# Performance work log

Measured on AMD Instinct MI355X. Metric: run time of the kernel, lower is better.

## Reference

```python
import jax, jax.numpy as jnp
import numpy as np

MARGIN = 0.2
EPS = 1e-12  # guards sqrt(0) (self-distance diagonal); sqrt(1e-12)=1e-6, negligible


def setup_inputs() -> dict:
    key = jax.random.key(0)
    n, m, d = 62, 256, 256          # parts, batch (32 ids x 8 samples), feat dim
    k_per_class = 8                 # positives per anchor (incl. self)
    feature = jax.random.normal(key, (n, m, d), dtype=jnp.float32)
    # structured labels required by the boolean_mask/reshape trick: equal counts per anchor
    label = jnp.broadcast_to(jnp.arange(m, dtype=jnp.int64) // k_per_class, (n, m))
    return {"feature": feature, "label": label, "num_pos": k_per_class}


def reference(feature, label, num_pos):
    n, m, d = feature.shape
    num_neg = m - num_pos
    hp_mask = label[:, :, None] == label[:, None, :]  # (n,m,m) same-id mask (incl. self)

    # batched pairwise euclidean distance
    x2 = jnp.sum(feature * feature, axis=2, keepdims=True)                   # (n,m,1)
    d2 = x2 + jnp.swapaxes(x2, 1, 2) - 2.0 * jnp.einsum('nid,njd->nij', feature, feature)
    dist = jnp.sqrt(jnp.maximum(d2, 0.0) + EPS)                              # (n,m,m)
    mean_dist = jnp.mean(dist)

    # stable argsort of mask: in-set entries (0) come first, in original column order,
    # exactly matching tf.boolean_mask row-major extraction + reshape.
    pos_idx = jnp.argsort((~hp_mask).astype(jnp.int32), axis=2)[:, :, :num_pos]
    neg_idx = jnp.argsort(hp_mask.astype(jnp.int32), axis=2)[:, :, :num_neg]
    pos_d = jnp.take_along_axis(dist, pos_idx, axis=2)  # (n,m,num_pos)
    neg_d = jnp.take_along_axis(dist, neg_idx, axis=2)  # (n,m,num_neg)

    # hard mining
    hard_loss = jax.nn.relu(MARGIN + jnp.max(pos_d, axis=2) - jnp.min(neg_d, axis=2))
    hard_loss_metric_mean = jnp.mean(hard_loss, axis=1)  # (n,)

    # full mining: all (pos, neg) pairs -> (n, m, num_pos, num_neg)
    full = jax.nn.relu(MARGIN + pos_d[:, :, :, None] - neg_d[:, :, None, :])
    full_sum = jnp.sum(full, axis=(1, 2))                                    # (n, num_neg)
    full_num = jnp.sum((full > 0).astype(jnp.float32), axis=(1, 2))          # (n, num_neg)
    full_mean = full_sum / (full_num + 1e-6)
    return (full_mean, hard_loss_metric_mean, mean_dist, full_num)
```

## Files before the change

kernel.cpp:

```cpp
#include <hip/hip_runtime.h>

#define NPART 62
#define M     256
#define DD    256
#define NPOS  8
#define NNEG  248
#define MARG  0.2f
#define REC   512

#define WS_NEED ((size_t)(496 * REC) * 4)

#define OFF_HARD 15376
#define OFF_MD   15438
#define OFF_FN   15439

typedef _Float16 f16x8 __attribute__((ext_vector_type(8)));
typedef float    f32x4 __attribute__((ext_vector_type(4)));

#define PITCH 258

__device__ __forceinline__ int fragpos(int r15, int g) { return (r15 ^ (g << 1)) + (g << 4); }

__global__ __launch_bounds__(1024) void k_all(const float* __restrict__ F,
                                              const int* __restrict__ label,
                                              float* __restrict__ recs)
{
    __shared__ __align__(16) char smem[64 * PITCH * 4];
    __shared__ float x2s[M];
    __shared__ float fullS[16][NNEG];
    __shared__ float fullC[16][NNEG];
    __shared__ float posbuf[16][NPOS];
    __shared__ float wred[32];

    const int bxr = blockIdx.x;
    const int swz = (bxr & 7) * 31 + (bxr >> 3);
    const int p   = swz >> 2;
    const int rt4 = swz & 3;
    const int ib  = rt4 * 64;
    const int a0  = rt4 * 4;
    const int t   = threadIdx.x;
    const int lane = t & 63;
    const int w    = t >> 6;

    const float* Fp = F + (size_t)p * (M * DD);

    const int srow = t >> 2;
    const int soct = t & 3;
    const int stile = srow >> 4;
    const int whalf = ((stile * 64) + fragpos(srow & 15, soct)) * 8;
    const float* gsrc = Fp + srow * DD + soct * 8;

    const int flane = fragpos(lane & 15, lane >> 4);

    _Float16* stage0 = (_Float16*)smem;
    _Float16* stage1 = (_Float16*)(smem + 16384);

    f32x4 acc[4];
#pragma unroll
    for (int rt = 0; rt < 4; ++rt) acc[rt] = (f32x4){0.f, 0.f, 0.f, 0.f};

    float x2p = 0.f;
    float4 v0, v1, n0, n1;

    auto CVT = [&](_Float16* SW, float4 a, float4 b) {
        float xx[8] = {a.x, a.y, a.z, a.w, b.x, b.y, b.z, b.w};
        f16x8 hv;
#pragma unroll
        for (int j = 0; j < 8; ++j) {
            x2p += xx[j] * xx[j];
            hv[j] = (_Float16)xx[j];
        }
        *(f16x8*)(SW + whalf) = hv;
    };

    v0 = *(const float4*)(gsrc + 0);
    v1 = *(const float4*)(gsrc + 4);
    CVT(stage0, v0, v1);
    __syncthreads();

#pragma unroll
    for (int s = 0; s < 8; ++s) {
        if (s < 7) {
            n0 = *(const float4*)(gsrc + (s + 1) * 32 + 0);
            n1 = *(const float4*)(gsrc + (s + 1) * 32 + 4);
        }
        const _Float16* SB = (s & 1) ? stage1 : stage0;
        {
            f16x8 B = *(const f16x8*)(SB + (w * 64 + flane) * 8);
#pragma unroll
            for (int rt = 0; rt < 4; ++rt) {
                f16x8 A = *(const f16x8*)(SB + ((a0 + rt) * 64 + flane) * 8);
                acc[rt] = __builtin_amdgcn_mfma_f32_16x16x32_f16(A, B, acc[rt], 0, 0, 0);
            }
        }
        if (s < 7) {
            CVT((s & 1) ? stage0 : stage1, n0, n1);
            __syncthreads();
        }
    }

    x2p += __shfl_xor(x2p, 1);
    x2p += __shfl_xor(x2p, 2);
    if ((lane & 3) == 0) x2s[srow] = x2p;
    __syncthreads();

    float* region = (float*)smem;
    const int cbase = lane & 15;
    const int rbase = (lane >> 4) * 4;
    const float xj = x2s[w * 16 + cbase];
#pragma unroll
    for (int rt = 0; rt < 4; ++rt)
#pragma unroll
        for (int r = 0; r < 4; ++r) {
            float xi = x2s[ib + rt * 16 + rbase + r];
            float d2 = xi + xj - 2.f * acc[rt][r];
            float dd = sqrtf(fmaxf(d2, 0.f) + 1e-12f);
            region[(rt * 16 + rbase + r) * PITCH + w * 16 + cbase] = dd;
        }
    __syncthreads();

    int llab[4];
#pragma unroll
    for (int ch = 0; ch < 4; ++ch) llab[ch] = label[p * M + ch * 64 + lane];

    for (int idx = lane; idx < NNEG; idx += 64) { fullS[w][idx] = 0.f; fullC[w][idx] = 0.f; }

    const unsigned long long lmask = (1ull << lane) - 1ull;
    float hardAcc = 0.f, rowSum = 0.f;

    for (int a = 0; a < 4; ++a) {
        const int ii = w * 4 + a;
        const int li = label[p * M + ib + ii];
        int runMatch = 0;
        float negmin = 3.4e38f;
        float ndv[4]; int nqv[4]; int nval[4];
#pragma unroll
        for (int ch = 0; ch < 4; ++ch) {
            const int j = ch * 64 + lane;
            float d = region[ii * PITCH + j];
            bool match = (llab[ch] == li);
            unsigned long long bal = __ballot(match);
            int posRank = runMatch + __popcll(bal & lmask);
            if (match) {
                if (posRank < NPOS) posbuf[w][posRank] = d;
                nval[ch] = 0; ndv[ch] = 0.f; nqv[ch] = 0;
            } else {
                ndv[ch] = d; nqv[ch] = j - posRank; nval[ch] = 1;
                negmin = fminf(negmin, d);
            }
            runMatch += __popcll(bal);
            rowSum += d;
        }
        asm volatile("s_waitcnt lgkmcnt(0)" ::: "memory");

        float maxpos = posbuf[w][0];
#pragma unroll
        for (int pp = 1; pp < NPOS; ++pp) maxpos = fmaxf(maxpos, posbuf[w][pp]);
#pragma unroll
        for (int off = 32; off >= 1; off >>= 1)
            negmin = fminf(negmin, __shfl_xor(negmin, off));
        hardAcc += fmaxf(MARG + maxpos - negmin, 0.f);

#pragma unroll
        for (int ch = 0; ch < 4; ++ch) {
            if (nval[ch]) {
                float dneg = ndv[ch]; int q = nqv[ch];
                float s = 0.f, cnt = 0.f;
#pragma unroll
                for (int pp = 0; pp < NPOS; ++pp) {
                    float v = MARG + posbuf[w][pp] - dneg;
                    if (v > 0.f) { s += v; cnt += 1.f; }
                }
                fullS[w][q] += s;
                fullC[w][q] += cnt;
            }
        }
    }

#pragma unroll
    for (int off = 32; off >= 1; off >>= 1) rowSum += __shfl_xor(rowSum, off);
    if (lane == 0) { wred[w] = hardAcc; wred[16 + w] = rowSum; }
    __syncthreads();

    float* rec = recs + (size_t)swz * REC;
    if (t < NNEG) {
        float s = 0.f, c = 0.f;
#pragma unroll
        for (int v = 0; v < 16; ++v) { s += fullS[v][t]; c += fullC[v][t]; }
        rec[t] = s;
        rec[NNEG + t] = c;
    }
    if (t == 0) {
        float h = 0.f, ds = 0.f;
#pragma unroll
        for (int v = 0; v < 16; ++v) { h += wred[v]; ds += wred[16 + v]; }
        rec[496] = h;
        rec[497] = ds;
    }
}

__global__ __launch_bounds__(256) void k_fin(const float* __restrict__ recs,
                                             float* __restrict__ out)
{
    const int p = blockIdx.x;
    const int t = threadIdx.x;
    if (p < NPART) {
        if (t < NNEG) {
            float s = 0.f, c = 0.f;
#pragma unroll
            for (int a = 0; a < 4; ++a) {
                const float* rec = recs + (size_t)(p * 4 + a) * REC;
                s += rec[t];
                c += rec[NNEG + t];
            }
            out[p * NNEG + t]          = s / (c + 1e-6f);
            out[OFF_FN + p * NNEG + t] = c;
        }
        if (t == 0) {
            float h = 0.f;
#pragma unroll
            for (int a = 0; a < 4; ++a) h += recs[(size_t)(p * 4 + a) * REC + 496];
            out[OFF_HARD + p] = h * (1.0f / 256.0f);
        }
    } else {
        __shared__ float red[4];
        float v = (t < 248) ? recs[(size_t)t * REC + 497] : 0.f;
#pragma unroll
        for (int off = 32; off >= 1; off >>= 1) v += __shfl_xor(v, off);
        if ((t & 63) == 0) red[t >> 6] = v;
        __syncthreads();
        if (t == 0)
            out[OFF_MD] = (red[0] + red[1] + red[2] + red[3]) / (float)((size_t)NPART * M * M);
    }
}

__global__ __launch_bounds__(256) void fb_main(
    const float* __restrict__ F, const int* __restrict__ label, float* __restrict__ ws)
{
    __shared__ __align__(16) float region[256 * 36];
    __shared__ float x2s[M];
    __shared__ int   lab[M];
    __shared__ float posbuf[4][NPOS];
    __shared__ float fullS[4][NNEG];
    __shared__ float fullC[4][NNEG];
    __shared__ float wred[8];

    const int bx = blockIdx.x;
    const int p  = bx >> 3;
    const int ib = (bx & 7) * 32;
    const int t  = threadIdx.x;

    lab[t] = label[p * M + t];
    for (int idx = t; idx < 4 * NNEG; idx += 256) {
        (&fullS[0][0])[idx] = 0.f;
        (&fullC[0][0])[idx] = 0.f;
    }
    __syncthreads();

    const float4* Fv = (const float4*)(F + (size_t)p * (M * DD));

    float acc[4][8];
#pragma unroll
    for (int r = 0; r < 4; ++r)
#pragma unroll
        for (int c = 0; c < 8; ++c) acc[r][c] = 0.f;

    float x2loc = 0.f;
    const int tc = t & 31;
    const int tg = t >> 5;

    for (int kt = 0; kt < 8; ++kt) {
#pragma unroll
        for (int w = 0; w < 8; ++w) {
            int ch = w * 256 + t;
            int r  = ch >> 3;
            int q  = ch & 7;
            float4 v = Fv[r * 64 + kt * 8 + q];
            float* dst = &region[r * 36 + q * 4];
            dst[0] = v.x; dst[1] = v.y; dst[2] = v.z; dst[3] = v.w;
        }
        __syncthreads();
#pragma unroll
        for (int k4 = 0; k4 < 8; ++k4) {
            float4 b = *(const float4*)&region[t * 36 + k4 * 4];
            x2loc += b.x * b.x + b.y * b.y + b.z * b.z + b.w * b.w;
        }
#pragma unroll
        for (int k4 = 0; k4 < 8; ++k4) {
            float4 a4[4], b4[8];
#pragma unroll
            for (int r = 0; r < 4; ++r)
                a4[r] = *(const float4*)&region[(ib + tg * 4 + r) * 36 + k4 * 4];
#pragma unroll
            for (int c = 0; c < 8; ++c)
                b4[c] = *(const float4*)&region[(tc + 32 * c) * 36 + k4 * 4];
#pragma unroll
            for (int r = 0; r < 4; ++r)
#pragma unroll
                for (int c = 0; c < 8; ++c)
                    acc[r][c] += a4[r].x * b4[c].x + a4[r].y * b4[c].y +
                                 a4[r].z * b4[c].z + a4[r].w * b4[c].w;
        }
        __syncthreads();
    }

    x2s[t] = x2loc;
    __syncthreads();

#pragma unroll
    for (int r = 0; r < 4; ++r) {
        int ii = tg * 4 + r;
        float xi = x2s[ib + ii];
#pragma unroll
        for (int c = 0; c < 8; ++c) {
            int j = tc + 32 * c;
            float d2 = xi + x2s[j] - 2.f * acc[r][c];
            region[ii * M + j] = sqrtf(fmaxf(d2, 0.f) + 1e-12f);
        }
    }
    __syncthreads();

    const int lane = t & 63;
    const int w    = t >> 6;
    const unsigned long long lmask = (1ull << lane) - 1ull;

    float hardAcc = 0.f;
    float rowSum  = 0.f;

    for (int a = 0; a < 8; ++a) {
        int ii = w * 8 + a;
        int li = lab[ib + ii];
        int runMatch = 0;
        float negmin = 3.4e38f;
        float ndv[4]; int nqv[4]; int nval[4];
#pragma unroll
        for (int ch = 0; ch < 4; ++ch) {
            int j = ch * 64 + lane;
            float d = region[ii * M + j];
            bool match = (lab[j] == li);
            unsigned long long bal = __ballot(match);
            int prefix  = __popcll(bal & lmask);
            int posRank = runMatch + prefix;
            if (match) {
                if (posRank < NPOS) posbuf[w][posRank] = d;
                nval[ch] = 0; ndv[ch] = 0.f; nqv[ch] = 0;
            } else {
                ndv[ch] = d; nqv[ch] = j - posRank; nval[ch] = 1;
                negmin = fminf(negmin, d);
            }
            runMatch += __popcll(bal);
            rowSum += d;
        }
        __syncthreads();

        float maxpos = posbuf[w][0];
#pragma unroll
        for (int pp = 1; pp < NPOS; ++pp) maxpos = fmaxf(maxpos, posbuf[w][pp]);
#pragma unroll
        for (int off = 32; off >= 1; off >>= 1)
            negmin = fminf(negmin, __shfl_xor(negmin, off));
        hardAcc += fmaxf(MARG + maxpos - negmin, 0.f);

#pragma unroll
        for (int ch = 0; ch < 4; ++ch) {
            if (nval[ch]) {
                float dneg = ndv[ch]; int q = nqv[ch];
                float s = 0.f, cnt = 0.f;
#pragma unroll
                for (int pp = 0; pp < NPOS; ++pp) {
                    float v = MARG + posbuf[w][pp] - dneg;
                    if (v > 0.f) { s += v; cnt += 1.f; }
                }
                fullS[w][q] += s;
                fullC[w][q] += cnt;
            }
        }
        __syncthreads();
    }

#pragma unroll
    for (int off = 32; off >= 1; off >>= 1) rowSum += __shfl_xor(rowSum, off);
    if (lane == 0) { wred[w] = hardAcc; wred[4 + w] = rowSum; }
    __syncthreads();

    float* rec = ws + (size_t)bx * REC;
    if (t < NNEG) {
        float s = fullS[0][t] + fullS[1][t] + fullS[2][t] + fullS[3][t];
        float c = fullC[0][t] + fullC[1][t] + fullC[2][t] + fullC[3][t];
        rec[t] = s;
        rec[NNEG + t] = c;
    }
    if (t == 0) {
        rec[496] = wred[0] + wred[1] + wred[2] + wred[3];
        rec[497] = wred[4] + wred[5] + wred[6] + wred[7];
    }
}

__global__ __launch_bounds__(256) void fb_fin(const float* __restrict__ recs,
                                              float* __restrict__ out)
{
    const int p = blockIdx.x;
    const int t = threadIdx.x;
    if (p < NPART) {
        if (t < NNEG) {
            float s = 0.f, c = 0.f;
            for (int a = 0; a < 8; ++a) {
                const float* rec = recs + (size_t)(p * 8 + a) * REC;
                s += rec[t];
                c += rec[NNEG + t];
            }
            out[p * NNEG + t]          = s / (c + 1e-6f);
            out[OFF_FN + p * NNEG + t] = c;
        }
        if (t == 0) {
            float h = 0.f;
            for (int a = 0; a < 8; ++a) h += recs[(size_t)(p * 8 + a) * REC + 496];
            out[OFF_HARD + p] = h * (1.0f / 256.0f);
        }
    } else {
        __shared__ float red[4];
        float v = 0.f;
        for (int i = t; i < 496; i += 256) v += recs[(size_t)i * REC + 497];
#pragma unroll
        for (int off = 32; off >= 1; off >>= 1) v += __shfl_xor(v, off);
        if ((t & 63) == 0) red[t >> 6] = v;
        __syncthreads();
        if (t == 0)
            out[OFF_MD] = (red[0] + red[1] + red[2] + red[3]) / (float)((size_t)NPART * M * M);
    }
}

extern "C" void kernel_launch(void* const* d_in, const int* in_sizes, int n_in,
                              void* d_out, int out_size, void* d_ws, size_t ws_size,
                              hipStream_t stream)
{
    const float* F     = (const float*)d_in[0];
    const int*   label = (const int*)d_in[1];
    float*       ws    = (float*)d_ws;
    float*       out   = (float*)d_out;

    if (ws_size >= WS_NEED) {
        k_all<<<dim3(248), dim3(1024), 0, stream>>>(F, label, ws);
        k_fin<<<dim3(63),  dim3(256),  0, stream>>>(ws, out);
    } else {
        fb_main<<<dim3(496), dim3(256), 0, stream>>>(F, label, ws);
        fb_fin <<<dim3(63),  dim3(256), 0, stream>>>(ws, out);
    }
}
```

Baseline: 23.53 us.

## Double K-chunk per pipeline stage and move distance sum to epilogue

The staged GEMM loop now loads and converts two 32-wide K chunks per stage, so there are 4 stages instead of 8 and half as many barriers. Stage buffers move to a larger offset. The mean-distance partial sum is now computed while distances are written in the epilogue, rather than re-read during mining. The per-positive branch in full mining is replaced with branchless fmax/select. In exchange it uses more shared memory and more registers for the prefetched loads.

```diff
diff --git a/kernel.cpp b/kernel.cpp
--- a/kernel.cpp
+++ b/kernel.cpp
@@ -53,16 +53,15 @@
     const int flane = fragpos(lane & 15, lane >> 4);
 
     _Float16* stage0 = (_Float16*)smem;
-    _Float16* stage1 = (_Float16*)(smem + 16384);
+    _Float16* stage1 = (_Float16*)(smem + 32768);
 
     f32x4 acc[4];
 #pragma unroll
     for (int rt = 0; rt < 4; ++rt) acc[rt] = (f32x4){0.f, 0.f, 0.f, 0.f};
 
     float x2p = 0.f;
-    float4 v0, v1, n0, n1;
-
-    auto CVT = [&](_Float16* SW, float4 a, float4 b) {
+
+    auto CVT = [&](_Float16* SW, float4 a, float4 b, int u) {
         float xx[8] = {a.x, a.y, a.z, a.w, b.x, b.y, b.z, b.w};
         f16x8 hv;
 #pragma unroll
@@ -70,31 +69,44 @@
             x2p += xx[j] * xx[j];
             hv[j] = (_Float16)xx[j];
         }
-        *(f16x8*)(SW + whalf) = hv;
+        *(f16x8*)(SW + u * 8192 + whalf) = hv;
     };
 
-    v0 = *(const float4*)(gsrc + 0);
-    v1 = *(const float4*)(gsrc + 4);
-    CVT(stage0, v0, v1);
-    __syncthreads();
-
-#pragma unroll
-    for (int s = 0; s < 8; ++s) {
-        if (s < 7) {
-            n0 = *(const float4*)(gsrc + (s + 1) * 32 + 0);
-            n1 = *(const float4*)(gsrc + (s + 1) * 32 + 4);
-        }
-        const _Float16* SB = (s & 1) ? stage1 : stage0;
-        {
-            f16x8 B = *(const f16x8*)(SB + (w * 64 + flane) * 8);
+    {
+        float4 a0v = *(const float4*)(gsrc + 0);
+        float4 a1v = *(const float4*)(gsrc + 4);
+        float4 b0v = *(const float4*)(gsrc + 32);
+        float4 b1v = *(const float4*)(gsrc + 36);
+        CVT(stage0, a0v, a1v, 0);
+        CVT(stage0, b0v, b1v, 1);
+    }
+    __syncthreads();
+
+#pragma unroll
+    for (int P = 0; P < 4; ++P) {
+        float4 m0, m1, m2, m3;
+        if (P < 3) {
+            const float* g = gsrc + (P + 1) * 64;
+            m0 = *(const float4*)(g + 0);
+            m1 = *(const float4*)(g + 4);
+            m2 = *(const float4*)(g + 32);
+            m3 = *(const float4*)(g + 36);
+        }
+        const _Float16* SB = (P & 1) ? stage1 : stage0;
+#pragma unroll
+        for (int u = 0; u < 2; ++u) {
+            const _Float16* SU = SB + u * 8192;
+            f16x8 B = *(const f16x8*)(SU + (w * 64 + flane) * 8);
 #pragma unroll
             for (int rt = 0; rt < 4; ++rt) {
-                f16x8 A = *(const f16x8*)(SB + ((a0 + rt) * 64 + flane) * 8);
+                f16x8 A = *(const f16x8*)(SU + ((a0 + rt) * 64 + flane) * 8);
                 acc[rt] = __builtin_amdgcn_mfma_f32_16x16x32_f16(A, B, acc[rt], 0, 0, 0);
             }
         }
-        if (s < 7) {
-            CVT((s & 1) ? stage0 : stage1, n0, n1);
+        if (P < 3) {
+            _Float16* SW = (P & 1) ? stage0 : stage1;
+            CVT(SW, m0, m1, 0);
+            CVT(SW, m2, m3, 1);
             __syncthreads();
         }
     }
@@ -108,6 +120,7 @@
     const int cbase = lane & 15;
     const int rbase = (lane >> 4) * 4;
     const float xj = x2s[w * 16 + cbase];
+    float dsum = 0.f;
 #pragma unroll
     for (int rt = 0; rt < 4; ++rt)
 #pragma unroll
@@ -115,8 +128,12 @@
             float xi = x2s[ib + rt * 16 + rbase + r];
             float d2 = xi + xj - 2.f * acc[rt][r];
             float dd = sqrtf(fmaxf(d2, 0.f) + 1e-12f);
+            dsum += dd;
             region[(rt * 16 + rbase + r) * PITCH + w * 16 + cbase] = dd;
         }
+#pragma unroll
+    for (int off = 32; off >= 1; off >>= 1) dsum += __shfl_xor(dsum, off);
+    if (lane == 0) wred[16 + w] = dsum;
     __syncthreads();
 
     int llab[4];
@@ -126,7 +143,7 @@
     for (int idx = lane; idx < NNEG; idx += 64) { fullS[w][idx] = 0.f; fullC[w][idx] = 0.f; }
 
     const unsigned long long lmask = (1ull << lane) - 1ull;
-    float hardAcc = 0.f, rowSum = 0.f;
+    float hardAcc = 0.f;
 
     for (int a = 0; a < 4; ++a) {
         const int ii = w * 4 + a;
@@ -149,7 +166,6 @@
                 negmin = fminf(negmin, d);
             }
             runMatch += __popcll(bal);
-            rowSum += d;
         }
         asm volatile("s_waitcnt lgkmcnt(0)" ::: "memory");
 
@@ -169,7 +185,8 @@
 #pragma unroll
                 for (int pp = 0; pp < NPOS; ++pp) {
                     float v = MARG + posbuf[w][pp] - dneg;
-                    if (v > 0.f) { s += v; cnt += 1.f; }
+                    s   += fmaxf(v, 0.f);
+                    cnt += (v > 0.f) ? 1.f : 0.f;
                 }
                 fullS[w][q] += s;
                 fullC[w][q] += cnt;
@@ -177,9 +194,7 @@
         }
     }
 
-#pragma unroll
-    for (int off = 32; off >= 1; off >>= 1) rowSum += __shfl_xor(rowSum, off);
-    if (lane == 0) { wred[w] = hardAcc; wred[16 + w] = rowSum; }
+    if (lane == 0) wred[w] = hardAcc;
     __syncthreads();
 
     float* rec = recs + (size_t)swz * REC;
```

Result: no change. 23.18 us (-1.5%).
